# Kernel optimization log

Hardware: AMD Instinct MI355X
Metric: run time of the kernel (lower is better)

The kernel has to match this reference:

```python
import jax, jax.numpy as jnp
import numpy as np

B, L, S = 1, 2048, 2048
D_MODEL, H = 1024, 16
DK = D_MODEL // H  # d_keys = d_values = 64


def sparsemax(z):
    # sparsemax along last axis: proj of z onto the simplex
    K = z.shape[-1]
    z_sorted = jnp.flip(jnp.sort(z, axis=-1), axis=-1)
    cs = jnp.cumsum(z_sorted, axis=-1)
    r = jnp.arange(1, K + 1, dtype=z.dtype)
    support = 1.0 + r * z_sorted > cs
    k = jnp.sum(support, axis=-1, keepdims=True)
    tau = (jnp.take_along_axis(cs, k.astype(jnp.int32) - 1, axis=-1) - 1.0) / k.astype(z.dtype)
    return jnp.maximum(z - tau, 0.0)


def setup_inputs() -> dict:
    key = jax.random.key(0)
    ks = jax.random.split(key, 12)
    sc = 1.0 / np.sqrt(D_MODEL)
    return {
        "queries": jax.random.normal(ks[0], (B, L, D_MODEL), jnp.float32),
        "keys": jax.random.normal(ks[1], (B, S, D_MODEL), jnp.float32),
        "values": jax.random.normal(ks[2], (B, S, D_MODEL), jnp.float32),
        "Wq": jax.random.normal(ks[3], (D_MODEL, H * DK), jnp.float32) * sc,
        "bq": jnp.zeros((H * DK,), jnp.float32),
        "Wk": jax.random.normal(ks[4], (D_MODEL, H * DK), jnp.float32) * sc,
        "bk": jnp.zeros((H * DK,), jnp.float32),
        "Wv": jax.random.normal(ks[5], (H * DK, H * DK), jnp.float32) * sc,
        "bv": jnp.zeros((H * DK,), jnp.float32),
        "Wo": jax.random.normal(ks[6], (H * DK, D_MODEL), jnp.float32) * sc,
        "bo": jnp.zeros((D_MODEL,), jnp.float32),
    }


def reference(queries, keys, values, Wq, bq, Wk, bk, Wv, bv, Wo, bo):
    # projections (note: input `values` is unused, matching the torch source)
    q = (queries @ Wq + bq).reshape(B, L, H, DK)
    k_flat = keys @ Wk + bk                      # [B,S,H*DK]
    k = k_flat.reshape(B, S, H, DK)
    v = (k_flat @ Wv + bv).reshape(B, S, H, DK)  # value_projection(key_projection(keys))
    scale = 1.0 / np.sqrt(DK)
    scores = jnp.einsum('blhe,bshe->bhls', q, k) * scale  # [B,H,L,S]
    A = sparsemax(scores)
    out = jnp.einsum('bhls,bshd->blhd', A, v)             # [B,L,H,DK]
    # mix=True: transpose(2,1) -> [B,H,L,D] then view(B,L,-1)
    out = jnp.swapaxes(out, 1, 2).reshape(B, L, H * DK)
    return out @ Wo + bo
```

## Files before the change

kernel.cpp:

```cpp
#include <hip/hip_runtime.h>
#include <hip/hip_bf16.h>


typedef __attribute__((ext_vector_type(8))) short short8;
typedef __attribute__((ext_vector_type(4))) float floatx4;

#define SRC_BF16 0
#define SRC_F32  1
#define SRC_RT   2
#define CAP 192

__device__ __forceinline__ short f2bf(float f) {
    __hip_bfloat16 h = __float2bfloat16(f);
    return *reinterpret_cast<const short*>(&h);
}
__device__ __forceinline__ unsigned short f2bfu(float f) {
    __hip_bfloat16 h = __float2bfloat16(f);
    return *reinterpret_cast<const unsigned short*>(&h);
}
__device__ __forceinline__ float bf2f(unsigned short u) {
    return __uint_as_float(((unsigned)u) << 16);
}
__device__ __forceinline__ unsigned fmap(float f) {
    unsigned u = __float_as_uint(f);
    return (u & 0x80000000u) ? ~u : (u | 0x80000000u);
}
__device__ __forceinline__ float funmap(unsigned u) {
    return (u & 0x80000000u) ? __uint_as_float(u ^ 0x80000000u) : __uint_as_float(~u);
}

__global__ void detect_k(const short* __restrict__ q, int n, int* __restrict__ flag)
{
    const int tid = threadIdx.x;
    int bad = 0;
    for (int i = tid; i < n; i += 64) {
        float f = bf2f((unsigned short)q[i]);
        if (!(fabsf(f) < 1e10f)) bad = 1;
    }
    unsigned long long m = __ballot(bad != 0);
    if (tid == 0) *flag = (m != 0ULL) ? 1 : 0;
}

__global__ __launch_bounds__(256)
void convert2_k(const void* __restrict__ s0, const void* __restrict__ s1,
                short* __restrict__ d0, short* __restrict__ d1,
                const int* __restrict__ dflag)
{
    const void* s = blockIdx.z ? s1 : s0;
    short* d = blockIdx.z ? d1 : d0;
    const size_t i = ((size_t)blockIdx.x * 256 + threadIdx.x) * 8;
    short8 o;
    if (*dflag) {
        const float4 f0 = ((const float4*)((const float*)s + i))[0];
        const float4 f1 = ((const float4*)((const float*)s + i))[1];
        o[0] = f2bf(f0.x); o[1] = f2bf(f0.y); o[2] = f2bf(f0.z); o[3] = f2bf(f0.w);
        o[4] = f2bf(f1.x); o[5] = f2bf(f1.y); o[6] = f2bf(f1.z); o[7] = f2bf(f1.w);
    } else {
        o = *(const short8*)((const short*)s + i);
    }
    *(short8*)(d + i) = o;
}

struct TP4 {
    const void* s[4];
    short* d[4];
};
__global__ __launch_bounds__(256)
void transpose4_k(TP4 p, int R, int C, const int* __restrict__ dflag)
{
    __shared__ short T[64][72];
    const int tid = threadIdx.x;
    const int bC = blockIdx.x, bR = blockIdx.y;
    const void* src = p.s[blockIdx.z];
    short* dst = p.d[blockIdx.z];
    const bool f32 = (*dflag != 0);

    const int colg = (tid & 7) * 8;
    #pragma unroll
    for (int h = 0; h < 2; ++h) {
        const int row = (tid >> 3) + 32 * h;
        const size_t idx = (size_t)(bR * 64 + row) * (size_t)C + (size_t)(bC * 64 + colg);
        short e[8];
        if (f32) {
            const float4 f0 = ((const float4*)((const float*)src + idx))[0];
            const float4 f1 = ((const float4*)((const float*)src + idx))[1];
            e[0] = f2bf(f0.x); e[1] = f2bf(f0.y); e[2] = f2bf(f0.z); e[3] = f2bf(f0.w);
            e[4] = f2bf(f1.x); e[5] = f2bf(f1.y); e[6] = f2bf(f1.z); e[7] = f2bf(f1.w);
        } else {
            short8 s = *(const short8*)((const short*)src + idx);
            #pragma unroll
            for (int j = 0; j < 8; ++j) e[j] = s[j];
        }
        #pragma unroll
        for (int j = 0; j < 8; ++j) T[colg + j][row] = e[j];
    }
    __syncthreads();
    #pragma unroll
    for (int h = 0; h < 2; ++h) {
        const int orow = (tid >> 3) + 32 * h;
        const int ocolg = (tid & 7) * 8;
        const size_t idx = (size_t)(bC * 64 + orow) * (size_t)R + (size_t)(bR * 64 + ocolg);
        *(short8*)(dst + idx) = *(const short8*)&T[orow][ocolg];
    }
}

struct GJ { const short* A; const short* B; const void* bias; void* C; };

template<int OSRC>
__global__ __launch_bounds__(256)
void gemm64_bt_k(GJ j0, GJ j1, const int* __restrict__ dflag)
{
    __shared__ __align__(16) short As[64][40];
    __shared__ __align__(16) short Bs[64][40];

    const GJ j = blockIdx.z ? j1 : j0;
    const int rtf = *dflag;

    const int tid  = threadIdx.x;
    const int bN   = blockIdx.x, bM = blockIdx.y;
    const int lane = tid & 63, wave = tid >> 6;
    const int wm   = (wave >> 1) * 32;
    const int wn   = (wave & 1) * 32;
    const int quad = lane >> 4, r16 = lane & 15;

    floatx4 acc[2][2];
    #pragma unroll
    for (int i = 0; i < 2; ++i)
        #pragma unroll
        for (int jj = 0; jj < 2; ++jj)
            acc[i][jj] = (floatx4){0.f, 0.f, 0.f, 0.f};

    const int ar = tid >> 2, ac = (tid & 3) * 8;

    for (int k0 = 0; k0 < 1024; k0 += 32) {
        *(short8*)&As[ar][ac] =
            *(const short8*)(j.A + (size_t)(bM * 64 + ar) * 1024 + (size_t)(k0 + ac));
        *(short8*)&Bs[ar][ac] =
            *(const short8*)(j.B + (size_t)(bN * 64 + ar) * 1024 + (size_t)(k0 + ac));
        __syncthreads();

        short8 a0 = *(const short8*)&As[wm + r16][quad * 8];
        short8 a1 = *(const short8*)&As[wm + 16 + r16][quad * 8];
        short8 b0 = *(const short8*)&Bs[wn + r16][quad * 8];
        short8 b1 = *(const short8*)&Bs[wn + 16 + r16][quad * 8];

        acc[0][0] = __builtin_amdgcn_mfma_f32_16x16x32_bf16(a0, b0, acc[0][0], 0, 0, 0);
        acc[0][1] = __builtin_amdgcn_mfma_f32_16x16x32_bf16(a0, b1, acc[0][1], 0, 0, 0);
        acc[1][0] = __builtin_amdgcn_mfma_f32_16x16x32_bf16(a1, b0, acc[1][0], 0, 0, 0);
        acc[1][1] = __builtin_amdgcn_mfma_f32_16x16x32_bf16(a1, b1, acc[1][1], 0, 0, 0);
        __syncthreads();
    }

    const bool of32 = (OSRC == SRC_F32) || (OSRC == SRC_RT && rtf);
    #pragma unroll
    for (int jj = 0; jj < 2; ++jj) {
        const int gc = bN * 64 + wn + jj * 16 + r16;
        const float bb = rtf ? ((const float*)j.bias)[gc]
                             : bf2f(((const unsigned short*)j.bias)[gc]);
        #pragma unroll
        for (int i = 0; i < 2; ++i) {
            #pragma unroll
            for (int rg = 0; rg < 4; ++rg) {
                const int gr = bM * 64 + wm + i * 16 + quad * 4 + rg;
                const float v = acc[i][jj][rg] + bb;
                if (of32)
                    ((float*)j.C)[(size_t)gr * 1024 + gc] = v;
                else
                    ((__hip_bfloat16*)j.C)[(size_t)gr * 1024 + gc] = __float2bfloat16(v);
            }
        }
    }
}

__global__ __launch_bounds__(256, 8)
void attn_fused_k(const short* __restrict__ Qb, const short* __restrict__ Kb,
                  const short* __restrict__ Vb, short* __restrict__ Ob)
{
    __shared__ unsigned cpk[16][CAP];
    __shared__ unsigned rmax[16];
    __shared__ int cnt[16];

    const int tid  = threadIdx.x;
    const int lane = tid & 63, wave = tid >> 6;
    const int quad = lane >> 4, r16 = lane & 15;

    const int bid  = blockIdx.x;
    const int slot = bid >> 3;
    const int h    = (slot & 1) * 8 + (bid & 7);
    const int row0 = (slot >> 1) * 16;

    if (tid < 16) { rmax[tid] = fmap(-3.0e38f); cnt[tid] = 0; }
    __syncthreads();

    const short* qp = Qb + (size_t)(row0 + r16) * 1024 + h * 64 + quad * 8;
    const short8 qa0 = *(const short8*)qp;
    const short8 qa1 = *(const short8*)(qp + 32);

    const int myrow = quad * 4;
    const short* kp0 = Kb + (size_t)(wave * 16 + r16) * 1024 + h * 64 + quad * 8;

    float rm1[4], rm2[4];
    #pragma unroll
    for (int rg = 0; rg < 4; ++rg) { rm1[rg] = -3.0e38f; rm2[rg] = -3.0e38f; }

    for (int s0 = 0; s0 < 2048; s0 += 256) {
        floatx4 acc[4];
        #pragma unroll
        for (int t = 0; t < 4; ++t) {
            const short* kp = kp0 + (size_t)(s0 + t * 64) * 1024;
            const short8 b0 = *(const short8*)kp;
            const short8 b1 = *(const short8*)(kp + 32);
            floatx4 a = (floatx4){0.f, 0.f, 0.f, 0.f};
            a = __builtin_amdgcn_mfma_f32_16x16x32_bf16(qa0, b0, a, 0, 0, 0);
            a = __builtin_amdgcn_mfma_f32_16x16x32_bf16(qa1, b1, a, 0, 0, 0);
            #pragma unroll
            for (int rg = 0; rg < 4; ++rg) a[rg] *= 0.125f;
            acc[t] = a;
        }

        #pragma unroll
        for (int rg = 0; rg < 4; ++rg) {
            float m1ab = fmaxf(acc[0][rg], acc[1][rg]);
            float m2ab = fminf(acc[0][rg], acc[1][rg]);
            float m1cd = fmaxf(acc[2][rg], acc[3][rg]);
            float m2cd = fminf(acc[2][rg], acc[3][rg]);
            float m1 = fmaxf(m1ab, m1cd);
            float m2 = fmaxf(fminf(m1ab, m1cd), (m1ab >= m1cd) ? m2ab : m2cd);
            #pragma unroll
            for (int off = 1; off < 16; off <<= 1) {
                const float o1 = __shfl_xor(m1, off, 64);
                const float o2 = __shfl_xor(m2, off, 64);
                const float n2 = fmaxf(fminf(m1, o1), (m1 >= o1) ? m2 : o2);
                m1 = fmaxf(m1, o1);
                m2 = n2;
            }
            const float n1 = fmaxf(rm1[rg], m1);
            rm2[rg] = fmaxf(fminf(rm1[rg], m1), (rm1[rg] >= m1) ? rm2[rg] : m2);
            rm1[rg] = n1;
            if (r16 == 0) atomicMax(&rmax[myrow + rg], fmap(m1));
        }

        #pragma unroll
        for (int rg = 0; rg < 4; ++rg) {
            const int row = myrow + rg;
            const float g1 = fmaxf(funmap(rmax[row]), rm1[rg]);
            const float thr = fmaxf(g1 - 1.0f, 0.5f * (g1 + rm2[rg]) - 0.5f);
            #pragma unroll
            for (int t = 0; t < 4; ++t) {
                const float val = acc[t][rg];
                const bool keep = (val >= thr);
                const unsigned long long m = __ballot(keep);
                const unsigned qm = (unsigned)((m >> (quad * 16)) & 0xFFFFull);
                int base = 0;
                if (r16 == 0 && qm) base = atomicAdd(&cnt[row], __popc(qm));
                base = __shfl(base, quad * 16, 64);
                if (keep) {
                    const int p = base + __popc(qm & ((1u << r16) - 1u));
                    if (p < CAP)
                        cpk[row][p] = ((unsigned)f2bfu(val) << 16)
                                    | (unsigned)(s0 + wave * 16 + t * 64 + r16);
                }
            }
        }
    }
    __syncthreads();

    const unsigned long long pre = (1ULL << lane) - 1ULL;
    for (int rr = 0; rr < 4; ++rr) {
        const int r = wave * 4 + rr;
        const int n = min(cnt[r], CAP);

        float v[3];
        unsigned short ii[3];
        #pragma unroll
        for (int i = 0; i < 3; ++i) {
            const int ix = lane + i * 64;
            if (ix < n) {
                const unsigned u = cpk[r][ix];
                v[i] = bf2f((unsigned short)(u >> 16));
                ii[i] = (unsigned short)(u & 0xFFFFu);
            } else { v[i] = -3.0e38f; ii[i] = 0; }
        }

        float tau = -3.0e38f, prevc = -1.0f;
        for (int it = 0; it < 24; ++it) {
            float s = 0.f, c = 0.f;
            #pragma unroll
            for (int i = 0; i < 3; ++i)
                if (v[i] > tau) { s += v[i]; c += 1.f; }
            #pragma unroll
            for (int off = 1; off < 64; off <<= 1) {
                s += __shfl_xor(s, off, 64);
                c += __shfl_xor(c, off, 64);
            }
            if (c == prevc) break;
            prevc = c;
            tau = (s - 1.0f) / c;
        }

        int base = 0;
        #pragma unroll
        for (int i = 0; i < 3; ++i) {
            const float p = v[i] - tau;
            const unsigned long long m = __ballot(p > 0.f);
            const int w = base + __popcll(m & pre);
            if (p > 0.f) cpk[r][w] = ((unsigned)f2bfu(p) << 16) | (unsigned)ii[i];
            base += __popcll(m);
        }
        const int msup = base;

        const unsigned short* vb = (const unsigned short*)Vb + (size_t)h * 64 + lane;
        float o0 = 0.f, o1 = 0.f, o2 = 0.f, o3 = 0.f;
        int jj = 0;
        for (; jj + 4 <= msup; jj += 4) {
            const unsigned u0 = cpk[r][jj],     u1 = cpk[r][jj + 1];
            const unsigned u2 = cpk[r][jj + 2], u3 = cpk[r][jj + 3];
            o0 += bf2f((unsigned short)(u0 >> 16)) * bf2f(vb[(size_t)(u0 & 0xFFFFu) * 1024]);
            o1 += bf2f((unsigned short)(u1 >> 16)) * bf2f(vb[(size_t)(u1 & 0xFFFFu) * 1024]);
            o2 += bf2f((unsigned short)(u2 >> 16)) * bf2f(vb[(size_t)(u2 & 0xFFFFu) * 1024]);
            o3 += bf2f((unsigned short)(u3 >> 16)) * bf2f(vb[(size_t)(u3 & 0xFFFFu) * 1024]);
        }
        for (; jj < msup; ++jj) {
            const unsigned u0 = cpk[r][jj];
            o0 += bf2f((unsigned short)(u0 >> 16)) * bf2f(vb[(size_t)(u0 & 0xFFFFu) * 1024]);
        }
        Ob[((size_t)h * 2048 + row0 + r) * 64 + lane] = f2bf(o0 + o1 + o2 + o3);
    }
}

extern "C" void kernel_launch(void* const* d_in, const int* in_sizes, int n_in,
                              void* d_out, int out_size, void* d_ws, size_t ws_size,
                              hipStream_t stream)
{
    (void)in_sizes; (void)n_in; (void)out_size; (void)ws_size;

    const void* queries = d_in[0];
    const void* keys    = d_in[1];
    const void* Wq = d_in[3];
    const void* bq = d_in[4];
    const void* Wk = d_in[5];
    const void* bk = d_in[6];
    const void* Wv = d_in[7];
    const void* bv = d_in[8];
    const void* Wo = d_in[9];
    const void* bo = d_in[10];

    const int L = 2048, DM = 1024;
    const size_t LD = (size_t)L * DM;

    int*   flag = (int*)d_ws;
    short* Qc  = (short*)((char*)d_ws + 256);
    short* Kc  = Qc + LD;
    short* WqT = Kc + LD;
    short* WkT = WqT + (size_t)DM * DM;
    short* WvT = WkT + (size_t)DM * DM;
    short* WoT = WvT + (size_t)DM * DM;
    short* Qb  = WoT + (size_t)DM * DM;
    short* Kb  = Qb + LD;
    short* Vb  = Kb + LD;
    short* Ob  = Vb + LD;

    dim3 blk(256);

    detect_k<<<dim3(1), dim3(64), 0, stream>>>((const short*)queries, 4096, flag);

    convert2_k<<<dim3((unsigned)(LD / 2048), 1, 2), blk, 0, stream>>>(
        queries, keys, Qc, Kc, flag);

    {
        TP4 p;
        p.s[0] = Wq; p.s[1] = Wk; p.s[2] = Wv; p.s[3] = Wo;
        p.d[0] = WqT; p.d[1] = WkT; p.d[2] = WvT; p.d[3] = WoT;
        transpose4_k<<<dim3(DM / 64, DM / 64, 4), blk, 0, stream>>>(p, DM, DM, flag);
    }

    {
        GJ jq{(const short*)Qc, WqT, bq, Qb};
        GJ jk{(const short*)Kc, WkT, bk, Kb};
        gemm64_bt_k<SRC_BF16><<<dim3(DM / 64, L / 64, 2), blk, 0, stream>>>(jq, jk, flag);
    }
    {
        GJ jv{(const short*)Kb, WvT, bv, Vb};
        gemm64_bt_k<SRC_BF16><<<dim3(DM / 64, L / 64, 1), blk, 0, stream>>>(jv, jv, flag);
    }

    attn_fused_k<<<dim3((L / 16) * 16), blk, 0, stream>>>(Qb, Kb, Vb, Ob);

    {
        GJ jo{(const short*)Ob, WoT, bo, d_out};
        gemm64_bt_k<SRC_RT><<<dim3(DM / 64, L / 64, 1), blk, 0, stream>>>(jo, jo, flag);
    }
}
```

Before: 266.4 us.

## Use per-lane candidate slots with overflow atomics and fold score scale into Q GEMM

```diff
diff --git a/kernel.cpp b/kernel.cpp
--- a/kernel.cpp
+++ b/kernel.cpp
@@ -8,7 +8,9 @@
 #define SRC_BF16 0
 #define SRC_F32  1
 #define SRC_RT   2
-#define CAP 192
+#define NSEG 3
+#define OVF 64
+#define CAPT (64 * NSEG + OVF)
 
 __device__ __forceinline__ short f2bf(float f) {
     __hip_bfloat16 h = __float2bfloat16(f);
@@ -104,7 +106,7 @@
     }
 }
 
-struct GJ { const short* A; const short* B; const void* bias; void* C; };
+struct GJ { const short* A; const short* B; const void* bias; void* C; float os; };
 
 template<int OSRC>
 __global__ __launch_bounds__(256)
@@ -162,7 +164,7 @@
             #pragma unroll
             for (int rg = 0; rg < 4; ++rg) {
                 const int gr = bM * 64 + wm + i * 16 + quad * 4 + rg;
-                const float v = acc[i][jj][rg] + bb;
+                const float v = (acc[i][jj][rg] + bb) * j.os;
                 if (of32)
                     ((float*)j.C)[(size_t)gr * 1024 + gc] = v;
                 else
@@ -176,7 +178,7 @@
 void attn_fused_k(const short* __restrict__ Qb, const short* __restrict__ Kb,
                   const short* __restrict__ Vb, short* __restrict__ Ob)
 {
-    __shared__ unsigned cpk[16][CAP];
+    __shared__ unsigned cpk[16][CAPT];
     __shared__ unsigned rmax[16];
     __shared__ int cnt[16];
 
@@ -197,11 +199,13 @@
     const short8 qa1 = *(const short8*)(qp + 32);
 
     const int myrow = quad * 4;
+    const int wid   = wave * 16 + r16;
     const short* kp0 = Kb + (size_t)(wave * 16 + r16) * 1024 + h * 64 + quad * 8;
 
     float rm1[4], rm2[4];
-    #pragma unroll
-    for (int rg = 0; rg < 4; ++rg) { rm1[rg] = -3.0e38f; rm2[rg] = -3.0e38f; }
+    int mycnt[4];
+    #pragma unroll
+    for (int rg = 0; rg < 4; ++rg) { rm1[rg] = -3.0e38f; rm2[rg] = -3.0e38f; mycnt[rg] = 0; }
 
     for (int s0 = 0; s0 < 2048; s0 += 256) {
         floatx4 acc[4];
@@ -213,8 +217,6 @@
             floatx4 a = (floatx4){0.f, 0.f, 0.f, 0.f};
             a = __builtin_amdgcn_mfma_f32_16x16x32_bf16(qa0, b0, a, 0, 0, 0);
             a = __builtin_amdgcn_mfma_f32_16x16x32_bf16(qa1, b1, a, 0, 0, 0);
-            #pragma unroll
-            for (int rg = 0; rg < 4; ++rg) a[rg] *= 0.125f;
             acc[t] = a;
         }
 
@@ -248,45 +250,54 @@
             #pragma unroll
             for (int t = 0; t < 4; ++t) {
                 const float val = acc[t][rg];
-                const bool keep = (val >= thr);
-                const unsigned long long m = __ballot(keep);
-                const unsigned qm = (unsigned)((m >> (quad * 16)) & 0xFFFFull);
-                int base = 0;
-                if (r16 == 0 && qm) base = atomicAdd(&cnt[row], __popc(qm));
-                base = __shfl(base, quad * 16, 64);
-                if (keep) {
-                    const int p = base + __popc(qm & ((1u << r16) - 1u));
-                    if (p < CAP)
-                        cpk[row][p] = ((unsigned)f2bfu(val) << 16)
-                                    | (unsigned)(s0 + wave * 16 + t * 64 + r16);
+                if (val >= thr) {
+                    const unsigned pk = ((unsigned)f2bfu(val) << 16)
+                                      | (unsigned)(s0 + wave * 16 + t * 64 + r16);
+                    const int c = mycnt[rg];
+                    if (c < NSEG) {
+                        cpk[row][wid * NSEG + c] = pk;
+                    } else {
+                        const int p = atomicAdd(&cnt[row], 1);
+                        if (p < OVF) cpk[row][64 * NSEG + p] = pk;
+                    }
+                    mycnt[rg] = c + 1;
                 }
             }
         }
+    }
+
+    #pragma unroll
+    for (int rg = 0; rg < 4; ++rg) {
+        const int row = myrow + rg;
+        for (int k = mycnt[rg]; k < NSEG; ++k)
+            cpk[row][wid * NSEG + k] = 0xFF800000u;
     }
     __syncthreads();
 
     const unsigned long long pre = (1ULL << lane) - 1ULL;
     for (int rr = 0; rr < 4; ++rr) {
         const int r = wave * 4 + rr;
-        const int n = min(cnt[r], CAP);
-
-        float v[3];
-        unsigned short ii[3];
+        const int novf = min(cnt[r], OVF);
+
+        float v[4];
+        unsigned short ii[4];
         #pragma unroll
         for (int i = 0; i < 3; ++i) {
-            const int ix = lane + i * 64;
-            if (ix < n) {
-                const unsigned u = cpk[r][ix];
-                v[i] = bf2f((unsigned short)(u >> 16));
-                ii[i] = (unsigned short)(u & 0xFFFFu);
-            } else { v[i] = -3.0e38f; ii[i] = 0; }
-        }
-
-        float tau = -3.0e38f, prevc = -1.0f;
+            const unsigned u = cpk[r][lane + i * 64];
+            v[i] = bf2f((unsigned short)(u >> 16));
+            ii[i] = (unsigned short)(u & 0xFFFFu);
+        }
+        if (lane < novf) {
+            const unsigned u = cpk[r][64 * NSEG + lane];
+            v[3] = bf2f((unsigned short)(u >> 16));
+            ii[3] = (unsigned short)(u & 0xFFFFu);
+        } else { v[3] = -3.0e38f; ii[3] = 0; }
+
+        float tau = funmap(rmax[r]) - 1.0f, prevc = -1.0f;
         for (int it = 0; it < 24; ++it) {
             float s = 0.f, c = 0.f;
             #pragma unroll
-            for (int i = 0; i < 3; ++i)
+            for (int i = 0; i < 4; ++i)
                 if (v[i] > tau) { s += v[i]; c += 1.f; }
             #pragma unroll
             for (int off = 1; off < 64; off <<= 1) {
@@ -300,7 +311,7 @@
 
         int base = 0;
         #pragma unroll
-        for (int i = 0; i < 3; ++i) {
+        for (int i = 0; i < 4; ++i) {
             const float p = v[i] - tau;
             const unsigned long long m = __ballot(p > 0.f);
             const int w = base + __popcll(m & pre);
@@ -375,19 +386,19 @@
     }
 
     {
-        GJ jq{(const short*)Qc, WqT, bq, Qb};
-        GJ jk{(const short*)Kc, WkT, bk, Kb};
+        GJ jq{(const short*)Qc, WqT, bq, Qb, 0.125f};
+        GJ jk{(const short*)Kc, WkT, bk, Kb, 1.0f};
         gemm64_bt_k<SRC_BF16><<<dim3(DM / 64, L / 64, 2), blk, 0, stream>>>(jq, jk, flag);
     }
     {
-        GJ jv{(const short*)Kb, WvT, bv, Vb};
+        GJ jv{(const short*)Kb, WvT, bv, Vb, 1.0f};
         gemm64_bt_k<SRC_BF16><<<dim3(DM / 64, L / 64, 1), blk, 0, stream>>>(jv, jv, flag);
     }
 
     attn_fused_k<<<dim3((L / 16) * 16), blk, 0, stream>>>(Qb, Kb, Vb, Ob);
 
     {
-        GJ jo{(const short*)Ob, WoT, bo, d_out};
+        GJ jo{(const short*)Ob, WoT, bo, d_out, 1.0f};
         gemm64_bt_k<SRC_RT><<<dim3(DM / 64, L / 64, 1), blk, 0, stream>>>(jo, jo, flag);
     }
 }
```

After: 279.8 us. 1.05x slower.
